# Performance work log

Measured on AMD Instinct MI355X. Metric: run time of the kernel, lower is better.

Reference implementation:

```python
import jax, jax.numpy as jnp
import numpy as np

# 5x5 scent diffusion kernel (hard-coded in torch source)
SCENT_K = jnp.array([[0.0, 0.125, 0.25, 0.125, 0.0],
                     [0.125, 0.25, 0.5, 0.25, 0.125],
                     [0.25, 0.5, 1.0, 0.5, 0.25],
                     [0.125, 0.25, 0.5, 0.25, 0.125],
                     [0.0, 0.125, 0.25, 0.125, 0.0]], dtype=jnp.float32)
# Sobel-like perception kernels
DX = jnp.outer(jnp.array([1.0, 2.0, 1.0]), jnp.array([-1.0, 0.0, 1.0])) / 8.0
DY = DX.T


def _maxpool3(x):  # x: (H, W); 3x3 maxpool, stride 1, SAME padding
    return jax.lax.reduce_window(x, -jnp.inf, jax.lax.max, (3, 3), (1, 1), 'SAME')


def _depthwise3(x, k):  # x: (4, H, W); same 3x3 kernel applied per channel
    # treat channels as batch: (4,1,H,W) conv (1,1,3,3)
    return jax.lax.conv_general_dilated(x[:, None], k[None, None].astype(x.dtype),
                                        (1, 1), 'SAME')[:, 0]


def _update(cell, food, w3, b3, w4, b4):
    # scent: 5x5 conv on food (note: torch mutates cell[3] in place before masking)
    scent = jax.lax.conv_general_dilated(food[None, None], SCENT_K[None, None],
                                         (1, 1), 'SAME')[0, 0]
    cell = cell.at[3].set(scent)
    pre_alive = _maxpool3(cell[0]) > 0.1
    # perceive: (4 + 4 + 4) = 12 channels
    y = jnp.concatenate([cell, _depthwise3(cell, DX), _depthwise3(cell, DY)], axis=0)
    h = jax.nn.relu(jnp.einsum('oc,chw->ohw', w3, y) + b3[:, None, None])
    delta = jnp.einsum('oc,chw->ohw', w4, h) + b4[:, None, None]
    x = cell + delta
    post_alive = _maxpool3(x[0]) > 0.1
    mask = (pre_alive & post_alive).astype(x.dtype)
    x = x * mask
    x = x.at[3].set(cell[3])  # restore scent channel
    return jnp.clip(x, -10.0, 10.0)


def setup_inputs() -> dict:
    key = jax.random.key(0)
    k1, k2, k3, k4 = jax.random.split(key, 4)
    return {
        'cell': jax.random.normal(k1, (4, 17, 17), dtype=jnp.float32),
        'food': jax.random.uniform(k2, (17, 17), dtype=jnp.float32),
        'w3': jax.random.normal(k3, (16, 12), dtype=jnp.float32) * 0.1,
        'b3': jnp.zeros((16,), dtype=jnp.float32),
        'w4': jax.random.normal(k4, (4, 16), dtype=jnp.float32) * 0.1,
        'b4': jnp.zeros((4,), dtype=jnp.float32),
        'steps': 256,
    }


def reference(cell, food, w3, b3, w4, b4, steps):
    def step(c, _):
        return _update(c, food, w3, b3, w4, b4), None
    cell, _ = jax.lax.scan(step, cell, None, length=steps)
    living_count = jnp.sum(cell[0])
    return cell, food, living_count
```

## Files before the change

### kernel.cpp

```cpp
#include <hip/hip_runtime.h>

namespace {

constexpr int H = 17, W = 17, NC = H * W;
constexpr int SW = 20, SH = 19;
constexpr int NT = 320;

#define PIN(x) asm volatile("" : "+v"(x))

__device__ __forceinline__ float clip10(float v) {
    return fminf(fmaxf(v, -10.f), 10.f);
}

__device__ __forceinline__ float max3f(float a, float b, float c) {
    return fmaxf(fmaxf(a, b), c);
}

__device__ __forceinline__ float scent_at(int hy, int wx, const float* __restrict__ food) {
    const float SK[5][5] = {
        {0.f,   .125f, .25f, .125f, 0.f},
        {.125f, .25f,  .5f,  .25f,  .125f},
        {.25f,  .5f,   1.f,  .5f,   .25f},
        {.125f, .25f,  .5f,  .25f,  .125f},
        {0.f,   .125f, .25f, .125f, 0.f}};
    float sc = 0.f;
    #pragma unroll
    for (int dy = -2; dy <= 2; ++dy) {
        #pragma unroll
        for (int dx = -2; dx <= 2; ++dx) {
            const float k = SK[dy + 2][dx + 2];
            if (k != 0.f) {
                const int yy = hy + dy, xx = wx + dx;
                if (yy >= 0 && yy < H && xx >= 0 && xx < W)
                    sc = fmaf(k, food[yy * W + xx], sc);
            }
        }
    }
    return sc;
}

__launch_bounds__(NT, 2)
__global__ void ca_kernel(const float* __restrict__ cell_in,
                          const float* __restrict__ food,
                          const float* __restrict__ w3,
                          const float* __restrict__ b3,
                          const float* __restrict__ w4,
                          const float* __restrict__ b4,
                          const int* __restrict__ steps_p,
                          float* __restrict__ out)
{
    __shared__ float2 c01[SH * SW];
    __shared__ float  c2s[SH * SW];
    __shared__ float  scs[SH * SW];
    __shared__ float  xb[SH * SW];
    __shared__ float4 wlds[48];
    __shared__ float  red[NT];

    const int tid = (int)threadIdx.x;
    const int steps = steps_p[0];
    const bool act = tid < NC;

    for (int i = tid; i < SH * SW; i += NT) {
        c01[i] = make_float2(0.f, 0.f);
        c2s[i] = 0.f; scs[i] = 0.f; xb[i] = 0.f;
    }
    if (tid < 16) {
        const int o = tid;
        wlds[3*o]   = make_float4(w3[o*12+0], w3[o*12+1], w3[o*12+2], w3[o*12+4]*0.125f);
        wlds[3*o+1] = make_float4(w3[o*12+5]*0.125f, w3[o*12+6]*0.125f,
                                  w3[o*12+8]*0.125f, w3[o*12+9]*0.125f);
        wlds[3*o+2] = make_float4(w3[o*12+10]*0.125f, w4[o], w4[16+o], w4[32+o]);
    }
    __syncthreads();

    const int hy = act ? tid / W : 0;
    const int wx = act ? tid % W : 0;
    const int idx = (hy + 1) * SW + wx + 1;

    float cur0 = 0.f, cur1 = 0.f, cur2 = 0.f, sc = 0.f;
    if (act) {
        cur0 = cell_in[tid];
        cur1 = cell_in[NC + tid];
        cur2 = cell_in[2 * NC + tid];
        sc   = scent_at(hy, wx, food);
        c01[idx] = make_float2(cur0, cur1);
        c2s[idx] = cur2;
        scs[idx] = sc;
    }
    __syncthreads();

    float be[16];
    {
        const float s00 = scs[idx-SW-1], s01 = scs[idx-SW], s02 = scs[idx-SW+1];
        const float s10 = scs[idx-1],                       s12 = scs[idx+1];
        const float s20 = scs[idx+SW-1], s21 = scs[idx+SW], s22 = scs[idx+SW+1];
        const float dxs = ((s02-s00) + 2.f*(s12-s10) + (s22-s20)) * 0.125f;
        const float dys = ((s20+2.f*s21+s22) - (s00+2.f*s01+s02)) * 0.125f;
        #pragma unroll
        for (int o = 0; o < 16; ++o)
            be[o] = fmaf(w3[o*12+3], sc, fmaf(w3[o*12+7], dxs,
                    fmaf(w3[o*12+11], dys, b3[o])));
    }
    float b40 = b4[0], b41 = b4[1], b42 = b4[2];
    #pragma unroll
    for (int o = 0; o < 16; ++o) PIN(be[o]);
    PIN(b40); PIN(b41); PIN(b42);

    for (int s = 0; s < steps; ++s) {
        float n0 = 0.f, n1 = 0.f, n2 = 0.f;
        bool pre = false;
        if (act) {
            const float2 a00 = c01[idx-SW-1], a01 = c01[idx-SW], a02 = c01[idx-SW+1];
            const float2 a10 = c01[idx-1],                       a12 = c01[idx+1];
            const float2 a20 = c01[idx+SW-1], a21 = c01[idx+SW], a22 = c01[idx+SW+1];
            const float r00 = c2s[idx-SW-1], r01 = c2s[idx-SW], r02 = c2s[idx-SW+1];
            const float r10 = c2s[idx-1],                       r12 = c2s[idx+1];
            const float r20 = c2s[idx+SW-1], r21 = c2s[idx+SW], r22 = c2s[idx+SW+1];

            const float y0 = cur0, y1 = cur1, y2 = cur2;
            const float y3 = (a02.x-a00.x) + 2.f*(a12.x-a10.x) + (a22.x-a20.x);
            const float y4 = (a02.y-a00.y) + 2.f*(a12.y-a10.y) + (a22.y-a20.y);
            const float y5 = (r02-r00) + 2.f*(r12-r10) + (r22-r20);
            const float y6 = (a20.x+2.f*a21.x+a22.x) - (a00.x+2.f*a01.x+a02.x);
            const float y7 = (a20.y+2.f*a21.y+a22.y) - (a00.y+2.f*a01.y+a02.y);
            const float y8 = (r20+2.f*r21+r22) - (r00+2.f*r01+r02);
            pre = max3f(max3f(a00.x,a01.x,a02.x), max3f(a10.x,cur0,a12.x),
                        max3f(a20.x,a21.x,a22.x)) > 0.1f;

            float d0 = b40, d1 = b41, d2 = b42;
            #pragma unroll
            for (int o = 0; o < 16; ++o) {
                const float4 wa = wlds[3*o], wb = wlds[3*o+1], wc = wlds[3*o+2];
                float a = be[o];
                a = fmaf(wa.x, y0, a); a = fmaf(wa.y, y1, a);
                a = fmaf(wa.z, y2, a); a = fmaf(wa.w, y3, a);
                a = fmaf(wb.x, y4, a); a = fmaf(wb.y, y5, a);
                a = fmaf(wb.z, y6, a); a = fmaf(wb.w, y7, a);
                a = fmaf(wc.x, y8, a);
                a = fmaxf(a, 0.f);
                d0 = fmaf(wc.y, a, d0);
                d1 = fmaf(wc.z, a, d1);
                d2 = fmaf(wc.w, a, d2);
            }
            n0 = y0 + d0; n1 = y1 + d1; n2 = y2 + d2;
            xb[idx] = n0;
        }
        __syncthreads();
        if (act) {
            const float x00 = xb[idx-SW-1], x01 = xb[idx-SW], x02 = xb[idx-SW+1];
            const float x10 = xb[idx-1],                      x12 = xb[idx+1];
            const float x20 = xb[idx+SW-1], x21 = xb[idx+SW], x22 = xb[idx+SW+1];
            const float mx2 = max3f(max3f(x00,x01,x02), max3f(x10,n0,x12),
                                    max3f(x20,x21,x22));
            const float m = (pre && (mx2 > 0.1f)) ? 1.f : 0.f;
            cur0 = clip10(n0 * m);
            cur1 = clip10(n1 * m);
            cur2 = clip10(n2 * m);
            c01[idx] = make_float2(cur0, cur1);
            c2s[idx] = cur2;
        }
        __syncthreads();
    }

    if (act) {
        out[tid]          = cur0;
        out[NC + tid]     = cur1;
        out[2 * NC + tid] = cur2;
        out[3 * NC + tid] = clip10(sc);
        out[4 * NC + tid] = food[tid];
        red[tid] = cur0;
    } else {
        red[tid] = 0.f;
    }
    __syncthreads();
    if (tid < 64) {
        float s2 = red[tid] + red[tid + 64] + red[tid + 128]
                 + red[tid + 192] + red[tid + 256];
        #pragma unroll
        for (int off = 32; off > 0; off >>= 1)
            s2 += __shfl_down(s2, off, 64);
        if (tid == 0) out[5 * NC] = s2;
    }
}

}

extern "C" void kernel_launch(void* const* d_in, const int* in_sizes, int n_in,
                              void* d_out, int out_size, void* d_ws, size_t ws_size,
                              hipStream_t stream) {
    const float* cell = (const float*)d_in[0];
    const float* food = (const float*)d_in[1];
    const float* w3   = (const float*)d_in[2];
    const float* b3   = (const float*)d_in[3];
    const float* w4   = (const float*)d_in[4];
    const float* b4   = (const float*)d_in[5];
    const int*   st   = (const int*)d_in[6];
    float* out = (float*)d_out;
    ca_kernel<<<1, NT, 0, stream>>>(cell, food, w3, b3, w4, b4, st, out);
}
```

Measured before the change: 355.3 us.

## Stream packed weights from global memory with pipelined inline-asm loads

A separate prep kernel packs and pre-scales the MLP weights and b4 into a workspace buffer. The main kernel now reloads them every step with uniform global_load_dwordx4 instructions in two double-buffered register banks, using explicit vmcnt waits. Per-thread bias terms move from pinned registers to LDS. The intent is to replace LDS weight reads and lower register pressure, but it adds global/L2 load latency on the serial per-step critical path and a second kernel launch.

```diff
diff --git a/kernel.cpp b/kernel.cpp
--- a/kernel.cpp
+++ b/kernel.cpp
@@ -1,17 +1,16 @@
 #include <hip/hip_runtime.h>
 
 namespace {
+
+typedef float f32x4 __attribute__((ext_vector_type(4)));
 
 constexpr int H = 17, W = 17, NC = H * W;
 constexpr int SW = 20, SH = 19;
 constexpr int NT = 320;
 
-#define PIN(x) asm volatile("" : "+v"(x))
-
 __device__ __forceinline__ float clip10(float v) {
     return fminf(fmaxf(v, -10.f), 10.f);
 }
-
 __device__ __forceinline__ float max3f(float a, float b, float c) {
     return fmaxf(fmaxf(a, b), c);
 }
@@ -39,37 +38,75 @@
     return sc;
 }
 
+#define GLD4(dst, OFFSTR) \
+    asm volatile("global_load_dwordx4 %0, %1, off offset:" OFFSTR \
+                 : "=v"(dst) : "v"(wbase))
+#define VWAIT(NSTR) do { \
+    asm volatile("s_waitcnt vmcnt(" NSTR ")" ::: "memory"); \
+    __builtin_amdgcn_sched_barrier(0); } while (0)
+
+#define DO_O(WA, WB, WC, BEV) do {                                    \
+    float a_ = (BEV);                                                 \
+    a_ = fmaf((WA).x, y0, a_); a_ = fmaf((WA).y, y1, a_);             \
+    a_ = fmaf((WA).z, y2, a_); a_ = fmaf((WA).w, y3, a_);             \
+    a_ = fmaf((WB).x, y4, a_); a_ = fmaf((WB).y, y5, a_);             \
+    a_ = fmaf((WB).z, y6, a_); a_ = fmaf((WB).w, y7, a_);             \
+    a_ = fmaf((WC).x, y8, a_);                                        \
+    a_ = fmaxf(a_, 0.f);                                              \
+    d0 = fmaf((WC).y, a_, d0); d1 = fmaf((WC).z, a_, d1);             \
+    d2 = fmaf((WC).w, a_, d2);                                        \
+} while (0)
+
+#define ISSUE_A(O0,O1,O2,O3,O4,O5,O6,O7,O8,O9,O10,O11) do {           \
+    GLD4(a0,O0); GLD4(a1,O1); GLD4(a2,O2); GLD4(a3,O3);               \
+    GLD4(a4,O4); GLD4(a5,O5); GLD4(a6,O6); GLD4(a7,O7);               \
+    GLD4(a8,O8); GLD4(a9,O9); GLD4(a10,O10); GLD4(a11,O11); } while (0)
+#define ISSUE_B(O0,O1,O2,O3,O4,O5,O6,O7,O8,O9,O10,O11) do {           \
+    GLD4(b0,O0); GLD4(b1,O1); GLD4(b2,O2); GLD4(b3,O3);               \
+    GLD4(b4q,O4); GLD4(b5,O5); GLD4(b6,O6); GLD4(b7,O7);              \
+    GLD4(b8,O8); GLD4(b9,O9); GLD4(b10,O10); GLD4(b11,O11); } while (0)
+
+__global__ void prep_kernel(const float* __restrict__ w3,
+                            const float* __restrict__ w4,
+                            const float* __restrict__ b4,
+                            float* __restrict__ ws)
+{
+    const int o = (int)threadIdx.x;
+    f32x4* q = (f32x4*)ws;
+    if (o < 16) {
+        q[3*o]   = (f32x4){w3[o*12+0], w3[o*12+1], w3[o*12+2], w3[o*12+4]*0.125f};
+        q[3*o+1] = (f32x4){w3[o*12+5]*0.125f, w3[o*12+6]*0.125f,
+                           w3[o*12+8]*0.125f, w3[o*12+9]*0.125f};
+        q[3*o+2] = (f32x4){w3[o*12+10]*0.125f, w4[o], w4[16+o], w4[32+o]};
+    } else if (o == 16) {
+        q[48] = (f32x4){b4[0], b4[1], b4[2], 0.f};
+    }
+}
+
 __launch_bounds__(NT, 2)
 __global__ void ca_kernel(const float* __restrict__ cell_in,
                           const float* __restrict__ food,
                           const float* __restrict__ w3,
                           const float* __restrict__ b3,
-                          const float* __restrict__ w4,
-                          const float* __restrict__ b4,
                           const int* __restrict__ steps_p,
+                          const float* __restrict__ wq,
                           float* __restrict__ out)
 {
     __shared__ float2 c01[SH * SW];
     __shared__ float  c2s[SH * SW];
     __shared__ float  scs[SH * SW];
     __shared__ float  xb[SH * SW];
-    __shared__ float4 wlds[48];
+    __shared__ f32x4  be4v[4 * NT];
     __shared__ float  red[NT];
 
     const int tid = (int)threadIdx.x;
     const int steps = steps_p[0];
     const bool act = tid < NC;
+    const unsigned long long wbase = (unsigned long long)wq;
 
     for (int i = tid; i < SH * SW; i += NT) {
         c01[i] = make_float2(0.f, 0.f);
         c2s[i] = 0.f; scs[i] = 0.f; xb[i] = 0.f;
-    }
-    if (tid < 16) {
-        const int o = tid;
-        wlds[3*o]   = make_float4(w3[o*12+0], w3[o*12+1], w3[o*12+2], w3[o*12+4]*0.125f);
-        wlds[3*o+1] = make_float4(w3[o*12+5]*0.125f, w3[o*12+6]*0.125f,
-                                  w3[o*12+8]*0.125f, w3[o*12+9]*0.125f);
-        wlds[3*o+2] = make_float4(w3[o*12+10]*0.125f, w4[o], w4[16+o], w4[32+o]);
     }
     __syncthreads();
 
@@ -89,59 +126,73 @@
     }
     __syncthreads();
 
-    float be[16];
-    {
+    if (act) {
         const float s00 = scs[idx-SW-1], s01 = scs[idx-SW], s02 = scs[idx-SW+1];
         const float s10 = scs[idx-1],                       s12 = scs[idx+1];
         const float s20 = scs[idx+SW-1], s21 = scs[idx+SW], s22 = scs[idx+SW+1];
         const float dxs = ((s02-s00) + 2.f*(s12-s10) + (s22-s20)) * 0.125f;
         const float dys = ((s20+2.f*s21+s22) - (s00+2.f*s01+s02)) * 0.125f;
+        float bt[16];
         #pragma unroll
         for (int o = 0; o < 16; ++o)
-            be[o] = fmaf(w3[o*12+3], sc, fmaf(w3[o*12+7], dxs,
+            bt[o] = fmaf(w3[o*12+3], sc, fmaf(w3[o*12+7], dxs,
                     fmaf(w3[o*12+11], dys, b3[o])));
-    }
-    float b40 = b4[0], b41 = b4[1], b42 = b4[2];
-    #pragma unroll
-    for (int o = 0; o < 16; ++o) PIN(be[o]);
-    PIN(b40); PIN(b41); PIN(b42);
+        be4v[0*NT + tid] = (f32x4){bt[0],  bt[1],  bt[2],  bt[3]};
+        be4v[1*NT + tid] = (f32x4){bt[4],  bt[5],  bt[6],  bt[7]};
+        be4v[2*NT + tid] = (f32x4){bt[8],  bt[9],  bt[10], bt[11]};
+        be4v[3*NT + tid] = (f32x4){bt[12], bt[13], bt[14], bt[15]};
+    }
+    __syncthreads();
 
     for (int s = 0; s < steps; ++s) {
         float n0 = 0.f, n1 = 0.f, n2 = 0.f;
         bool pre = false;
         if (act) {
-            const float2 a00 = c01[idx-SW-1], a01 = c01[idx-SW], a02 = c01[idx-SW+1];
-            const float2 a10 = c01[idx-1],                       a12 = c01[idx+1];
-            const float2 a20 = c01[idx+SW-1], a21 = c01[idx+SW], a22 = c01[idx+SW+1];
+            f32x4 a0,a1,a2,a3,a4,a5,a6,a7,a8,a9,a10,a11, ab4;
+            f32x4 b0,b1,b2,b3q,b4q,b5,b6,b7,b8,b9,b10,b11;
+            ISSUE_A("0","16","32","48","64","80","96","112","128","144","160","176");
+            GLD4(ab4, "768");
+            GLD4(b0,"192"); GLD4(b1,"208"); GLD4(b2,"224"); GLD4(b3q,"240");
+            GLD4(b4q,"256"); GLD4(b5,"272"); GLD4(b6,"288"); GLD4(b7,"304");
+            GLD4(b8,"320"); GLD4(b9,"336"); GLD4(b10,"352"); GLD4(b11,"368");
+
+            const float2 t00 = c01[idx-SW-1], t01 = c01[idx-SW], t02 = c01[idx-SW+1];
+            const float2 t10 = c01[idx-1],                       t12 = c01[idx+1];
+            const float2 t20 = c01[idx+SW-1], t21 = c01[idx+SW], t22 = c01[idx+SW+1];
             const float r00 = c2s[idx-SW-1], r01 = c2s[idx-SW], r02 = c2s[idx-SW+1];
             const float r10 = c2s[idx-1],                       r12 = c2s[idx+1];
             const float r20 = c2s[idx+SW-1], r21 = c2s[idx+SW], r22 = c2s[idx+SW+1];
+            const f32x4 bev0 = be4v[0*NT + tid], bev1 = be4v[1*NT + tid];
+            const f32x4 bev2 = be4v[2*NT + tid], bev3 = be4v[3*NT + tid];
 
             const float y0 = cur0, y1 = cur1, y2 = cur2;
-            const float y3 = (a02.x-a00.x) + 2.f*(a12.x-a10.x) + (a22.x-a20.x);
-            const float y4 = (a02.y-a00.y) + 2.f*(a12.y-a10.y) + (a22.y-a20.y);
+            const float y3 = (t02.x-t00.x) + 2.f*(t12.x-t10.x) + (t22.x-t20.x);
+            const float y4 = (t02.y-t00.y) + 2.f*(t12.y-t10.y) + (t22.y-t20.y);
             const float y5 = (r02-r00) + 2.f*(r12-r10) + (r22-r20);
-            const float y6 = (a20.x+2.f*a21.x+a22.x) - (a00.x+2.f*a01.x+a02.x);
-            const float y7 = (a20.y+2.f*a21.y+a22.y) - (a00.y+2.f*a01.y+a02.y);
+            const float y6 = (t20.x+2.f*t21.x+t22.x) - (t00.x+2.f*t01.x+t02.x);
+            const float y7 = (t20.y+2.f*t21.y+t22.y) - (t00.y+2.f*t01.y+t02.y);
             const float y8 = (r20+2.f*r21+r22) - (r00+2.f*r01+r02);
-            pre = max3f(max3f(a00.x,a01.x,a02.x), max3f(a10.x,cur0,a12.x),
-                        max3f(a20.x,a21.x,a22.x)) > 0.1f;
-
-            float d0 = b40, d1 = b41, d2 = b42;
-            #pragma unroll
-            for (int o = 0; o < 16; ++o) {
-                const float4 wa = wlds[3*o], wb = wlds[3*o+1], wc = wlds[3*o+2];
-                float a = be[o];
-                a = fmaf(wa.x, y0, a); a = fmaf(wa.y, y1, a);
-                a = fmaf(wa.z, y2, a); a = fmaf(wa.w, y3, a);
-                a = fmaf(wb.x, y4, a); a = fmaf(wb.y, y5, a);
-                a = fmaf(wb.z, y6, a); a = fmaf(wb.w, y7, a);
-                a = fmaf(wc.x, y8, a);
-                a = fmaxf(a, 0.f);
-                d0 = fmaf(wc.y, a, d0);
-                d1 = fmaf(wc.z, a, d1);
-                d2 = fmaf(wc.w, a, d2);
-            }
+            pre = max3f(max3f(t00.x,t01.x,t02.x), max3f(t10.x,cur0,t12.x),
+                        max3f(t20.x,t21.x,t22.x)) > 0.1f;
+
+            VWAIT("12");
+            float d0 = ab4.x, d1 = ab4.y, d2 = ab4.z;
+            DO_O(a0,a1,a2, bev0.x); DO_O(a3,a4,a5, bev0.y);
+            DO_O(a6,a7,a8, bev0.z); DO_O(a9,a10,a11, bev0.w);
+            ISSUE_A("384","400","416","432","448","464","480","496","512","528","544","560");
+            VWAIT("12");
+            DO_O(b0,b1,b2, bev1.x); DO_O(b3q,b4q,b5, bev1.y);
+            DO_O(b6,b7,b8, bev1.z); DO_O(b9,b10,b11, bev1.w);
+            GLD4(b0,"576"); GLD4(b1,"592"); GLD4(b2,"608"); GLD4(b3q,"624");
+            GLD4(b4q,"640"); GLD4(b5,"656"); GLD4(b6,"672"); GLD4(b7,"688");
+            GLD4(b8,"704"); GLD4(b9,"720"); GLD4(b10,"736"); GLD4(b11,"752");
+            VWAIT("12");
+            DO_O(a0,a1,a2, bev2.x); DO_O(a3,a4,a5, bev2.y);
+            DO_O(a6,a7,a8, bev2.z); DO_O(a9,a10,a11, bev2.w);
+            VWAIT("0");
+            DO_O(b0,b1,b2, bev3.x); DO_O(b3q,b4q,b5, bev3.y);
+            DO_O(b6,b7,b8, bev3.z); DO_O(b9,b10,b11, bev3.w);
+
             n0 = y0 + d0; n1 = y1 + d1; n2 = y2 + d2;
             xb[idx] = n0;
         }
@@ -196,5 +247,7 @@
     const float* b4   = (const float*)d_in[5];
     const int*   st   = (const int*)d_in[6];
     float* out = (float*)d_out;
-    ca_kernel<<<1, NT, 0, stream>>>(cell, food, w3, b3, w4, b4, st, out);
-}
+    float* ws  = (float*)d_ws;
+    prep_kernel<<<1, 64, 0, stream>>>(w3, w4, b4, ws);
+    ca_kernel<<<1, NT, 0, stream>>>(cell, food, w3, b3, st, ws, out);
+}
```

After: 550.2 us. 54.9% more time.

## Split hidden units across two thread halves with register-resident weights

Applied to the files above, without the earlier changes.

Doubles the block to 640 threads so each cell is handled by two threads, each computing 8 of the 16 hidden units, with partial deltas exchanged through shared memory. Weights move from LDS float4 loads into per-thread registers, with the w4 weights placed in scalar registers, and the three cell channels are packed into one float4 shared array. The aim is to shorten the serial per-step critical path of the single-block kernel. In exchange it adds a third barrier per step and an LDS exchange, which may offset the halved FMA work.

```diff
diff --git a/kernel.cpp b/kernel.cpp
--- a/kernel.cpp
+++ b/kernel.cpp
@@ -1,17 +1,24 @@
 #include <hip/hip_runtime.h>
 
 namespace {
+
+typedef float f32x4 __attribute__((ext_vector_type(4)));
 
 constexpr int H = 17, W = 17, NC = H * W;
 constexpr int SW = 20, SH = 19;
-constexpr int NT = 320;
-
-#define PIN(x) asm volatile("" : "+v"(x))
+constexpr int HALF = 320;
+constexpr int NT = 640;
+
+#define PINV(x) asm volatile("" : "+v"(x))
+#define PINS(x) asm volatile("" : "+s"(x))
+
+__device__ __forceinline__ float to_sgpr(float v) {
+    return __uint_as_float(__builtin_amdgcn_readfirstlane(__float_as_uint(v)));
+}
 
 __device__ __forceinline__ float clip10(float v) {
     return fminf(fmaxf(v, -10.f), 10.f);
 }
-
 __device__ __forceinline__ float max3f(float a, float b, float c) {
     return fmaxf(fmaxf(a, b), c);
 }
@@ -49,47 +56,64 @@
                           const int* __restrict__ steps_p,
                           float* __restrict__ out)
 {
-    __shared__ float2 c01[SH * SW];
-    __shared__ float  c2s[SH * SW];
-    __shared__ float  scs[SH * SW];
-    __shared__ float  xb[SH * SW];
-    __shared__ float4 wlds[48];
-    __shared__ float  red[NT];
+    __shared__ f32x4 c012[SH * SW];
+    __shared__ float scs[SH * SW];
+    __shared__ float xb[SH * SW];
+    __shared__ f32x4 pd[NT];
+    __shared__ float red[NT];
 
     const int tid = (int)threadIdx.x;
     const int steps = steps_p[0];
-    const bool act = tid < NC;
+    const bool hi = tid >= HALF;
+    const int ct = hi ? tid - HALF : tid;
+    const bool act = ct < NC;
+    const int cc = act ? ct : 0;
 
     for (int i = tid; i < SH * SW; i += NT) {
-        c01[i] = make_float2(0.f, 0.f);
-        c2s[i] = 0.f; scs[i] = 0.f; xb[i] = 0.f;
-    }
-    if (tid < 16) {
-        const int o = tid;
-        wlds[3*o]   = make_float4(w3[o*12+0], w3[o*12+1], w3[o*12+2], w3[o*12+4]*0.125f);
-        wlds[3*o+1] = make_float4(w3[o*12+5]*0.125f, w3[o*12+6]*0.125f,
-                                  w3[o*12+8]*0.125f, w3[o*12+9]*0.125f);
-        wlds[3*o+2] = make_float4(w3[o*12+10]*0.125f, w4[o], w4[16+o], w4[32+o]);
+        c012[i] = (f32x4){0.f, 0.f, 0.f, 0.f};
+        scs[i] = 0.f; xb[i] = 0.f;
     }
     __syncthreads();
 
-    const int hy = act ? tid / W : 0;
-    const int wx = act ? tid % W : 0;
+    const int hy = cc / W, wx = cc % W;
     const int idx = (hy + 1) * SW + wx + 1;
 
     float cur0 = 0.f, cur1 = 0.f, cur2 = 0.f, sc = 0.f;
     if (act) {
-        cur0 = cell_in[tid];
-        cur1 = cell_in[NC + tid];
-        cur2 = cell_in[2 * NC + tid];
+        cur0 = cell_in[ct];
+        cur1 = cell_in[NC + ct];
+        cur2 = cell_in[2 * NC + ct];
         sc   = scent_at(hy, wx, food);
-        c01[idx] = make_float2(cur0, cur1);
-        c2s[idx] = cur2;
-        scs[idx] = sc;
+        if (!hi) {
+            c012[idx] = (f32x4){cur0, cur1, cur2, 0.f};
+            scs[idx] = sc;
+        }
     }
     __syncthreads();
 
-    float be[16];
+    const int ub = hi ? 8 : 0;
+    float wp[8][9], be[8];
+    float w40[8], w41[8], w42[8];
+    #pragma unroll
+    for (int j = 0; j < 8; ++j) {
+        const int o = ub + j;
+        wp[j][0] = w3[o*12 + 0];
+        wp[j][1] = w3[o*12 + 1];
+        wp[j][2] = w3[o*12 + 2];
+        wp[j][3] = w3[o*12 + 4] * 0.125f;
+        wp[j][4] = w3[o*12 + 5] * 0.125f;
+        wp[j][5] = w3[o*12 + 6] * 0.125f;
+        wp[j][6] = w3[o*12 + 8] * 0.125f;
+        wp[j][7] = w3[o*12 + 9] * 0.125f;
+        wp[j][8] = w3[o*12 + 10] * 0.125f;
+        w40[j] = to_sgpr(w4[ub + j]);
+        w41[j] = to_sgpr(w4[16 + ub + j]);
+        w42[j] = to_sgpr(w4[32 + ub + j]);
+    }
+    float b40 = hi ? 0.f : b4[0];
+    float b41 = hi ? 0.f : b4[1];
+    float b42 = hi ? 0.f : b4[2];
+
     {
         const float s00 = scs[idx-SW-1], s01 = scs[idx-SW], s02 = scs[idx-SW+1];
         const float s10 = scs[idx-1],                       s12 = scs[idx+1];
@@ -97,53 +121,62 @@
         const float dxs = ((s02-s00) + 2.f*(s12-s10) + (s22-s20)) * 0.125f;
         const float dys = ((s20+2.f*s21+s22) - (s00+2.f*s01+s02)) * 0.125f;
         #pragma unroll
-        for (int o = 0; o < 16; ++o)
-            be[o] = fmaf(w3[o*12+3], sc, fmaf(w3[o*12+7], dxs,
+        for (int j = 0; j < 8; ++j) {
+            const int o = ub + j;
+            be[j] = fmaf(w3[o*12+3], sc, fmaf(w3[o*12+7], dxs,
                     fmaf(w3[o*12+11], dys, b3[o])));
-    }
-    float b40 = b4[0], b41 = b4[1], b42 = b4[2];
+        }
+    }
+
     #pragma unroll
-    for (int o = 0; o < 16; ++o) PIN(be[o]);
-    PIN(b40); PIN(b41); PIN(b42);
+    for (int j = 0; j < 8; ++j) {
+        #pragma unroll
+        for (int c = 0; c < 9; ++c) PINV(wp[j][c]);
+        PINV(be[j]);
+        PINS(w40[j]); PINS(w41[j]); PINS(w42[j]);
+    }
 
     for (int s = 0; s < steps; ++s) {
-        float n0 = 0.f, n1 = 0.f, n2 = 0.f;
+        float d0 = b40, d1 = b41, d2 = b42;
         bool pre = false;
         if (act) {
-            const float2 a00 = c01[idx-SW-1], a01 = c01[idx-SW], a02 = c01[idx-SW+1];
-            const float2 a10 = c01[idx-1],                       a12 = c01[idx+1];
-            const float2 a20 = c01[idx+SW-1], a21 = c01[idx+SW], a22 = c01[idx+SW+1];
-            const float r00 = c2s[idx-SW-1], r01 = c2s[idx-SW], r02 = c2s[idx-SW+1];
-            const float r10 = c2s[idx-1],                       r12 = c2s[idx+1];
-            const float r20 = c2s[idx+SW-1], r21 = c2s[idx+SW], r22 = c2s[idx+SW+1];
+            const f32x4 t00 = c012[idx-SW-1], t01 = c012[idx-SW], t02 = c012[idx-SW+1];
+            const f32x4 t10 = c012[idx-1],                        t12 = c012[idx+1];
+            const f32x4 t20 = c012[idx+SW-1], t21 = c012[idx+SW], t22 = c012[idx+SW+1];
 
             const float y0 = cur0, y1 = cur1, y2 = cur2;
-            const float y3 = (a02.x-a00.x) + 2.f*(a12.x-a10.x) + (a22.x-a20.x);
-            const float y4 = (a02.y-a00.y) + 2.f*(a12.y-a10.y) + (a22.y-a20.y);
-            const float y5 = (r02-r00) + 2.f*(r12-r10) + (r22-r20);
-            const float y6 = (a20.x+2.f*a21.x+a22.x) - (a00.x+2.f*a01.x+a02.x);
-            const float y7 = (a20.y+2.f*a21.y+a22.y) - (a00.y+2.f*a01.y+a02.y);
-            const float y8 = (r20+2.f*r21+r22) - (r00+2.f*r01+r02);
-            pre = max3f(max3f(a00.x,a01.x,a02.x), max3f(a10.x,cur0,a12.x),
-                        max3f(a20.x,a21.x,a22.x)) > 0.1f;
-
-            float d0 = b40, d1 = b41, d2 = b42;
+            const float y3 = (t02.x-t00.x) + 2.f*(t12.x-t10.x) + (t22.x-t20.x);
+            const float y4 = (t02.y-t00.y) + 2.f*(t12.y-t10.y) + (t22.y-t20.y);
+            const float y5 = (t02.z-t00.z) + 2.f*(t12.z-t10.z) + (t22.z-t20.z);
+            const float y6 = (t20.x+2.f*t21.x+t22.x) - (t00.x+2.f*t01.x+t02.x);
+            const float y7 = (t20.y+2.f*t21.y+t22.y) - (t00.y+2.f*t01.y+t02.y);
+            const float y8 = (t20.z+2.f*t21.z+t22.z) - (t00.z+2.f*t01.z+t02.z);
+            pre = max3f(max3f(t00.x,t01.x,t02.x), max3f(t10.x,cur0,t12.x),
+                        max3f(t20.x,t21.x,t22.x)) > 0.1f;
+
             #pragma unroll
-            for (int o = 0; o < 16; ++o) {
-                const float4 wa = wlds[3*o], wb = wlds[3*o+1], wc = wlds[3*o+2];
-                float a = be[o];
-                a = fmaf(wa.x, y0, a); a = fmaf(wa.y, y1, a);
-                a = fmaf(wa.z, y2, a); a = fmaf(wa.w, y3, a);
-                a = fmaf(wb.x, y4, a); a = fmaf(wb.y, y5, a);
-                a = fmaf(wb.z, y6, a); a = fmaf(wb.w, y7, a);
-                a = fmaf(wc.x, y8, a);
+            for (int j = 0; j < 8; ++j) {
+                float a = be[j];
+                a = fmaf(wp[j][0], y0, a); a = fmaf(wp[j][1], y1, a);
+                a = fmaf(wp[j][2], y2, a); a = fmaf(wp[j][3], y3, a);
+                a = fmaf(wp[j][4], y4, a); a = fmaf(wp[j][5], y5, a);
+                a = fmaf(wp[j][6], y6, a); a = fmaf(wp[j][7], y7, a);
+                a = fmaf(wp[j][8], y8, a);
                 a = fmaxf(a, 0.f);
-                d0 = fmaf(wc.y, a, d0);
-                d1 = fmaf(wc.z, a, d1);
-                d2 = fmaf(wc.w, a, d2);
+                d0 = fmaf(w40[j], a, d0);
+                d1 = fmaf(w41[j], a, d1);
+                d2 = fmaf(w42[j], a, d2);
             }
-            n0 = y0 + d0; n1 = y1 + d1; n2 = y2 + d2;
-            xb[idx] = n0;
+            pd[tid] = (f32x4){d0, d1, d2, 0.f};
+        }
+        __syncthreads();
+        float n0 = 0.f, n1 = 0.f, n2 = 0.f;
+        if (act) {
+            const f32x4 pp = pd[hi ? tid - HALF : tid + HALF];
+            n0 = cur0 + d0 + pp.x;
+            n1 = cur1 + d1 + pp.y;
+            n2 = cur2 + d2 + pp.z;
+            if (!hi) xb[idx] = n0;
         }
         __syncthreads();
         if (act) {
@@ -156,26 +189,26 @@
             cur0 = clip10(n0 * m);
             cur1 = clip10(n1 * m);
             cur2 = clip10(n2 * m);
-            c01[idx] = make_float2(cur0, cur1);
-            c2s[idx] = cur2;
+            if (!hi) c012[idx] = (f32x4){cur0, cur1, cur2, 0.f};
         }
         __syncthreads();
     }
 
-    if (act) {
-        out[tid]          = cur0;
-        out[NC + tid]     = cur1;
-        out[2 * NC + tid] = cur2;
-        out[3 * NC + tid] = clip10(sc);
-        out[4 * NC + tid] = food[tid];
+    if (act && !hi) {
+        out[ct]          = cur0;
+        out[NC + ct]     = cur1;
+        out[2 * NC + ct] = cur2;
+        out[3 * NC + ct] = clip10(sc);
+        out[4 * NC + ct] = food[ct];
         red[tid] = cur0;
     } else {
         red[tid] = 0.f;
     }
     __syncthreads();
     if (tid < 64) {
-        float s2 = red[tid] + red[tid + 64] + red[tid + 128]
-                 + red[tid + 192] + red[tid + 256];
+        float s2 = 0.f;
+        #pragma unroll
+        for (int k = 0; k < 10; ++k) s2 += red[tid + 64 * k];
         #pragma unroll
         for (int off = 32; off > 0; off >>= 1)
             s2 += __shfl_down(s2, off, 64);
```

New measurement: 333.9 us. 1.06x faster.

## Move packed weights to global scalar loads via prep kernel and split LDS planes

Applied to the files above, without the earlier changes.

Adds a separate prep kernel that packs w3, w4 and b4 into a global workspace. The main loop now reads those weights through uniform global loads that can go to scalar registers and cache, instead of through LDS float4 reads. Cell channels 0 and 1 are stored as separate LDS planes rather than interleaved float2, which gives plain 32-bit stencil loads. The cost is an extra kernel launch, plus reliance on the compiler turning the uniform loads into scalar loads.

```diff
diff --git a/kernel.cpp b/kernel.cpp
--- a/kernel.cpp
+++ b/kernel.cpp
@@ -1,6 +1,8 @@
 #include <hip/hip_runtime.h>
 
 namespace {
+
+typedef float f32x4 __attribute__((ext_vector_type(4)));
 
 constexpr int H = 17, W = 17, NC = H * W;
 constexpr int SW = 20, SH = 19;
@@ -11,7 +13,6 @@
 __device__ __forceinline__ float clip10(float v) {
     return fminf(fmaxf(v, -10.f), 10.f);
 }
-
 __device__ __forceinline__ float max3f(float a, float b, float c) {
     return fmaxf(fmaxf(a, b), c);
 }
@@ -39,37 +40,51 @@
     return sc;
 }
 
+#define LOAD9(ARR, IDX, T)                                                        \
+    const float T##00 = ARR[(IDX)-SW-1], T##01 = ARR[(IDX)-SW], T##02 = ARR[(IDX)-SW+1], \
+                T##10 = ARR[(IDX)-1],    T##11 = ARR[(IDX)],    T##12 = ARR[(IDX)+1],    \
+                T##20 = ARR[(IDX)+SW-1], T##21 = ARR[(IDX)+SW], T##22 = ARR[(IDX)+SW+1];
+
+__global__ void prep_kernel(const float* __restrict__ w3,
+                            const float* __restrict__ w4,
+                            const float* __restrict__ b4,
+                            float* __restrict__ ws)
+{
+    const int o = (int)threadIdx.x;
+    f32x4* q = (f32x4*)ws;
+    if (o < 16) {
+        q[3*o]   = (f32x4){w3[o*12+0], w3[o*12+1], w3[o*12+2], w3[o*12+4]*0.125f};
+        q[3*o+1] = (f32x4){w3[o*12+5]*0.125f, w3[o*12+6]*0.125f,
+                           w3[o*12+8]*0.125f, w3[o*12+9]*0.125f};
+        q[3*o+2] = (f32x4){w3[o*12+10]*0.125f, w4[o], w4[16+o], w4[32+o]};
+    } else if (o == 16) {
+        q[48] = (f32x4){b4[0], b4[1], b4[2], 0.f};
+    }
+}
+
 __launch_bounds__(NT, 2)
 __global__ void ca_kernel(const float* __restrict__ cell_in,
                           const float* __restrict__ food,
                           const float* __restrict__ w3,
                           const float* __restrict__ b3,
-                          const float* __restrict__ w4,
-                          const float* __restrict__ b4,
                           const int* __restrict__ steps_p,
+                          const float* __restrict__ wq,
                           float* __restrict__ out)
 {
-    __shared__ float2 c01[SH * SW];
-    __shared__ float  c2s[SH * SW];
-    __shared__ float  scs[SH * SW];
-    __shared__ float  xb[SH * SW];
-    __shared__ float4 wlds[48];
-    __shared__ float  red[NT];
+    __shared__ float c0s[SH * SW];
+    __shared__ float c1s[SH * SW];
+    __shared__ float c2s[SH * SW];
+    __shared__ float scs[SH * SW];
+    __shared__ float xb[SH * SW];
+    __shared__ float red[NT];
 
     const int tid = (int)threadIdx.x;
     const int steps = steps_p[0];
     const bool act = tid < NC;
+    const f32x4* __restrict__ q = (const f32x4*)wq;
 
     for (int i = tid; i < SH * SW; i += NT) {
-        c01[i] = make_float2(0.f, 0.f);
-        c2s[i] = 0.f; scs[i] = 0.f; xb[i] = 0.f;
-    }
-    if (tid < 16) {
-        const int o = tid;
-        wlds[3*o]   = make_float4(w3[o*12+0], w3[o*12+1], w3[o*12+2], w3[o*12+4]*0.125f);
-        wlds[3*o+1] = make_float4(w3[o*12+5]*0.125f, w3[o*12+6]*0.125f,
-                                  w3[o*12+8]*0.125f, w3[o*12+9]*0.125f);
-        wlds[3*o+2] = make_float4(w3[o*12+10]*0.125f, w4[o], w4[16+o], w4[32+o]);
+        c0s[i] = 0.f; c1s[i] = 0.f; c2s[i] = 0.f; scs[i] = 0.f; xb[i] = 0.f;
     }
     __syncthreads();
 
@@ -83,7 +98,8 @@
         cur1 = cell_in[NC + tid];
         cur2 = cell_in[2 * NC + tid];
         sc   = scent_at(hy, wx, food);
-        c01[idx] = make_float2(cur0, cur1);
+        c0s[idx] = cur0;
+        c1s[idx] = cur1;
         c2s[idx] = cur2;
         scs[idx] = sc;
     }
@@ -91,56 +107,47 @@
 
     float be[16];
     {
-        const float s00 = scs[idx-SW-1], s01 = scs[idx-SW], s02 = scs[idx-SW+1];
-        const float s10 = scs[idx-1],                       s12 = scs[idx+1];
-        const float s20 = scs[idx+SW-1], s21 = scs[idx+SW], s22 = scs[idx+SW+1];
+        LOAD9(scs, idx, s)
         const float dxs = ((s02-s00) + 2.f*(s12-s10) + (s22-s20)) * 0.125f;
         const float dys = ((s20+2.f*s21+s22) - (s00+2.f*s01+s02)) * 0.125f;
         #pragma unroll
         for (int o = 0; o < 16; ++o)
-            be[o] = fmaf(w3[o*12+3], sc, fmaf(w3[o*12+7], dxs,
+            be[o] = fmaf(w3[o*12+3], s11, fmaf(w3[o*12+7], dxs,
                     fmaf(w3[o*12+11], dys, b3[o])));
     }
-    float b40 = b4[0], b41 = b4[1], b42 = b4[2];
     #pragma unroll
     for (int o = 0; o < 16; ++o) PIN(be[o]);
-    PIN(b40); PIN(b41); PIN(b42);
 
     for (int s = 0; s < steps; ++s) {
         float n0 = 0.f, n1 = 0.f, n2 = 0.f;
         bool pre = false;
         if (act) {
-            const float2 a00 = c01[idx-SW-1], a01 = c01[idx-SW], a02 = c01[idx-SW+1];
-            const float2 a10 = c01[idx-1],                       a12 = c01[idx+1];
-            const float2 a20 = c01[idx+SW-1], a21 = c01[idx+SW], a22 = c01[idx+SW+1];
-            const float r00 = c2s[idx-SW-1], r01 = c2s[idx-SW], r02 = c2s[idx-SW+1];
-            const float r10 = c2s[idx-1],                       r12 = c2s[idx+1];
-            const float r20 = c2s[idx+SW-1], r21 = c2s[idx+SW], r22 = c2s[idx+SW+1];
-
+            LOAD9(c0s, idx, p) LOAD9(c1s, idx, a) LOAD9(c2s, idx, r)
             const float y0 = cur0, y1 = cur1, y2 = cur2;
-            const float y3 = (a02.x-a00.x) + 2.f*(a12.x-a10.x) + (a22.x-a20.x);
-            const float y4 = (a02.y-a00.y) + 2.f*(a12.y-a10.y) + (a22.y-a20.y);
+            const float y3 = (p02-p00) + 2.f*(p12-p10) + (p22-p20);
+            const float y4 = (a02-a00) + 2.f*(a12-a10) + (a22-a20);
             const float y5 = (r02-r00) + 2.f*(r12-r10) + (r22-r20);
-            const float y6 = (a20.x+2.f*a21.x+a22.x) - (a00.x+2.f*a01.x+a02.x);
-            const float y7 = (a20.y+2.f*a21.y+a22.y) - (a00.y+2.f*a01.y+a02.y);
+            const float y6 = (p20+2.f*p21+p22) - (p00+2.f*p01+p02);
+            const float y7 = (a20+2.f*a21+a22) - (a00+2.f*a01+a02);
             const float y8 = (r20+2.f*r21+r22) - (r00+2.f*r01+r02);
-            pre = max3f(max3f(a00.x,a01.x,a02.x), max3f(a10.x,cur0,a12.x),
-                        max3f(a20.x,a21.x,a22.x)) > 0.1f;
-
-            float d0 = b40, d1 = b41, d2 = b42;
+            pre = max3f(max3f(p00,p01,p02), max3f(p10,cur0,p12),
+                        max3f(p20,p21,p22)) > 0.1f;
+
+            const f32x4 bq = q[48];
+            float d0 = bq.x, d1 = bq.y, d2 = bq.z;
             #pragma unroll
             for (int o = 0; o < 16; ++o) {
-                const float4 wa = wlds[3*o], wb = wlds[3*o+1], wc = wlds[3*o+2];
-                float a = be[o];
-                a = fmaf(wa.x, y0, a); a = fmaf(wa.y, y1, a);
-                a = fmaf(wa.z, y2, a); a = fmaf(wa.w, y3, a);
-                a = fmaf(wb.x, y4, a); a = fmaf(wb.y, y5, a);
-                a = fmaf(wb.z, y6, a); a = fmaf(wb.w, y7, a);
-                a = fmaf(wc.x, y8, a);
-                a = fmaxf(a, 0.f);
-                d0 = fmaf(wc.y, a, d0);
-                d1 = fmaf(wc.z, a, d1);
-                d2 = fmaf(wc.w, a, d2);
+                const f32x4 qa = q[3*o], qb = q[3*o+1], qc = q[3*o+2];
+                float h = be[o];
+                h = fmaf(qa.x, y0, h); h = fmaf(qa.y, y1, h);
+                h = fmaf(qa.z, y2, h); h = fmaf(qa.w, y3, h);
+                h = fmaf(qb.x, y4, h); h = fmaf(qb.y, y5, h);
+                h = fmaf(qb.z, y6, h); h = fmaf(qb.w, y7, h);
+                h = fmaf(qc.x, y8, h);
+                h = fmaxf(h, 0.f);
+                d0 = fmaf(qc.y, h, d0);
+                d1 = fmaf(qc.z, h, d1);
+                d2 = fmaf(qc.w, h, d2);
             }
             n0 = y0 + d0; n1 = y1 + d1; n2 = y2 + d2;
             xb[idx] = n0;
@@ -156,7 +163,8 @@
             cur0 = clip10(n0 * m);
             cur1 = clip10(n1 * m);
             cur2 = clip10(n2 * m);
-            c01[idx] = make_float2(cur0, cur1);
+            c0s[idx] = cur0;
+            c1s[idx] = cur1;
             c2s[idx] = cur2;
         }
         __syncthreads();
@@ -196,5 +204,7 @@
     const float* b4   = (const float*)d_in[5];
     const int*   st   = (const int*)d_in[6];
     float* out = (float*)d_out;
-    ca_kernel<<<1, NT, 0, stream>>>(cell, food, w3, b3, w4, b4, st, out);
-}
+    float* ws  = (float*)d_ws;
+    prep_kernel<<<1, 64, 0, stream>>>(w3, w4, b4, ws);
+    ca_kernel<<<1, NT, 0, stream>>>(cell, food, w3, b3, st, ws, out);
+}
```

New measurement: 329.4 us. 7.3% less time.
